# Kernel optimization log

Hardware: AMD Instinct MI355X
Metric: run time of the kernel (lower is better)

Reference implementation:

```python
import jax, jax.numpy as jnp
import numpy as np

D_MODEL = 1024
N_HEAD = 16
STRIDE = 16
HEAD_DIM = D_MODEL // N_HEAD
B, TQ, TK = 4, 2048, 8192
L = TK // STRIDE  # per-head key count (same for all heads since n_head <= stride and TK % stride == 0)


def setup_inputs() -> dict:
    key = jax.random.key(0)
    ks = jax.random.split(key, 12)
    w_scale = 0.02
    return {
        "q": jax.random.normal(ks[0], (B, TQ, D_MODEL), dtype=jnp.float32),
        "k": jax.random.normal(ks[1], (B, TK, D_MODEL), dtype=jnp.float32),
        "v": jax.random.normal(ks[2], (B, TK, D_MODEL), dtype=jnp.float32),
        "src_mask": jnp.ones((B, 1, 1, TK), dtype=jnp.int32),
        "w_q": jax.random.normal(ks[3], (D_MODEL, D_MODEL), dtype=jnp.float32) * w_scale,
        "b_q": jnp.zeros((D_MODEL,), dtype=jnp.float32),
        "w_k": jax.random.normal(ks[4], (D_MODEL, D_MODEL), dtype=jnp.float32) * w_scale,
        "b_k": jnp.zeros((D_MODEL,), dtype=jnp.float32),
        "w_v": jax.random.normal(ks[5], (D_MODEL, D_MODEL), dtype=jnp.float32) * w_scale,
        "b_v": jnp.zeros((D_MODEL,), dtype=jnp.float32),
        "w_o": jax.random.normal(ks[6], (D_MODEL, D_MODEL), dtype=jnp.float32) * w_scale,
        "b_o": jnp.zeros((D_MODEL,), dtype=jnp.float32),
    }


def reference(q, k, v, src_mask, w_q, b_q, w_k, b_k, w_v, b_v, w_o, b_o):
    # projections (torch Linear: x @ W.T + b)
    Q = (q @ w_q.T + b_q).reshape(B, TQ, N_HEAD, HEAD_DIM).transpose(0, 2, 1, 3)  # [B,H,Tq,D]
    K = (k @ w_k.T + b_k).reshape(B, TK, N_HEAD, HEAD_DIM).transpose(0, 2, 1, 3)  # [B,H,Tk,D]
    V = (v @ w_v.T + b_v).reshape(B, TK, N_HEAD, HEAD_DIM).transpose(0, 2, 1, 3)

    # HEPOS strided per-head key indices: head h attends to positions h, h+stride, ...
    idx = jnp.arange(N_HEAD)[:, None] + STRIDE * jnp.arange(L)[None, :]  # [H,L]
    gidx = idx[None, :, :, None]  # broadcastable over batch and head_dim
    Kh = jnp.take_along_axis(K, gidx, axis=2)  # [B,H,L,D]
    Vh = jnp.take_along_axis(V, gidx, axis=2)  # [B,H,L,D]

    scores = jnp.einsum("bhqd,bhld->bhql", Q, Kh) / jnp.sqrt(jnp.float32(HEAD_DIM))
    # gather per-head mask slice: src_mask [B,1,1,Tk] -> [B,H,1,L]
    mask_b = jnp.broadcast_to(src_mask, (B, N_HEAD, 1, TK))
    mask_h = jnp.take_along_axis(mask_b, idx[None, :, None, :], axis=3)  # [B,H,1,L]
    scores = jnp.where(mask_h == 0, jnp.float32(-1e9), scores)

    attn = jax.nn.softmax(scores, axis=-1)  # dropout is identity in eval mode
    out = jnp.einsum("bhql,bhld->bhqd", attn, Vh)  # [B,H,Tq,D]
    out = out.transpose(0, 2, 1, 3).reshape(B, TQ, D_MODEL)
    return out @ w_o.T + b_o
```

## Files before the change

kernel.cpp:

```cpp
#include <hip/hip_runtime.h>
#include <stdint.h>

#define NBATCH 4
#define TQ 2048
#define TKK 8192
#define DM 1024
#define HDIM 64
#define LLEN 512

typedef __bf16 bf16;
typedef __attribute__((ext_vector_type(4))) float f32x4;
typedef __attribute__((ext_vector_type(8))) __bf16 bf16x8;
typedef __attribute__((ext_vector_type(4))) __bf16 bf16x4;

typedef const __attribute__((address_space(1))) void* gas1_t;
typedef __attribute__((address_space(3))) void* las3_t;

__device__ __forceinline__ void gload_lds16(const void* g, void* l) {
  __builtin_amdgcn_global_load_lds((gas1_t)(uintptr_t)g, (las3_t)(uint32_t)(uintptr_t)l, 16, 0, 0);
}

__global__ void cast_f32_bf16(const float* __restrict__ src, bf16* __restrict__ dst, int n4) {
  int i = blockIdx.x * blockDim.x + threadIdx.x;
  int stride = gridDim.x * blockDim.x;
  for (; i < n4; i += stride) {
    float4 v = ((const float4*)src)[i];
    bf16x4 o;
    o[0] = (bf16)v.x; o[1] = (bf16)v.y; o[2] = (bf16)v.z; o[3] = (bf16)v.w;
    ((bf16x4*)dst)[i] = o;
  }
}

__global__ void build_maskf(const int* __restrict__ sm, float* __restrict__ mf) {
  int i = blockIdx.x * blockDim.x + threadIdx.x;
  int bh = i >> 9, l = i & 511;
  int b = bh >> 4, h = bh & 15;
  mf[i] = sm[b * TKK + h + 16 * l] ? 1.0f : 0.0f;
}

template<bool OUT_BF16>
__global__ __launch_bounds__(256) void gemm_bt_bias(
    const bf16* __restrict__ A, const bf16* __restrict__ Bm,
    const float* __restrict__ bias, void* __restrict__ Cout, float scale) {
  __shared__ bf16 As[128 * 64];
  __shared__ bf16 Bs[128 * 64];
  const int t = threadIdx.x;
  const int lane = t & 63, w = t >> 6;
  const int wm = w >> 1, wn = w & 1;
  const int m0 = blockIdx.y * 128, n0 = blockIdx.x * 128;
  const int c = lane & 15, g = lane >> 4;
  f32x4 acc[4][4] = {};
  for (int k0 = 0; k0 < DM; k0 += 64) {
    __syncthreads();
    #pragma unroll
    for (int i = 0; i < 4; ++i) {
      int chunk = i * 256 + t;
      int row = chunk >> 3, blk = chunk & 7;
      gload_lds16(A + (size_t)(m0 + row) * DM + k0 + blk * 8, As + chunk * 8);
      gload_lds16(Bm + (size_t)(n0 + row) * DM + k0 + blk * 8, Bs + chunk * 8);
    }
    __syncthreads();
    #pragma unroll
    for (int kk = 0; kk < 2; ++kk) {
      bf16x8 af[4], bfr[4];
      #pragma unroll
      for (int f = 0; f < 4; ++f)
        af[f] = *(const bf16x8*)(As + (wm * 64 + f * 16 + c) * 64 + kk * 32 + g * 8);
      #pragma unroll
      for (int f = 0; f < 4; ++f)
        bfr[f] = *(const bf16x8*)(Bs + (wn * 64 + f * 16 + c) * 64 + kk * 32 + g * 8);
      #pragma unroll
      for (int mi = 0; mi < 4; ++mi)
        #pragma unroll
        for (int ni = 0; ni < 4; ++ni)
          acc[mi][ni] = __builtin_amdgcn_mfma_f32_16x16x32_bf16(af[mi], bfr[ni], acc[mi][ni], 0, 0, 0);
    }
  }
  #pragma unroll
  for (int ni = 0; ni < 4; ++ni) {
    int n = n0 + wn * 64 + ni * 16 + c;
    float bv = bias[n];
    #pragma unroll
    for (int mi = 0; mi < 4; ++mi) {
      int m = m0 + wm * 64 + mi * 16 + g * 4;
      #pragma unroll
      for (int j = 0; j < 4; ++j) {
        float vv = (acc[mi][ni][j] + bv) * scale;
        if (OUT_BF16) ((bf16*)Cout)[(size_t)(m + j) * DM + n] = (bf16)vv;
        else          ((float*)Cout)[(size_t)(m + j) * DM + n] = vv;
      }
    }
  }
}

template<int TRANSPOSE>
__global__ __launch_bounds__(256) void kv_proj(
    const float* __restrict__ X, const bf16* __restrict__ W,
    const float* __restrict__ bias, bf16* __restrict__ Out) {
  __shared__ bf16 As[128 * 64];
  __shared__ bf16 Bs[64 * 64];
  const int t = threadIdx.x, lane = t & 63, w = t >> 6;
  const int wm = w >> 1, wn = w & 1;
  const int bh = blockIdx.y, b = bh >> 4, h = bh & 15;
  const int l0 = blockIdx.x * 128;
  const int c = lane & 15, g = lane >> 4;
  f32x4 acc[4][2] = {};
  for (int k0 = 0; k0 < DM; k0 += 64) {
    __syncthreads();
    #pragma unroll
    for (int i = 0; i < 8; ++i) {
      int chunk = i * 256 + t;
      int row = chunk >> 4, q4 = chunk & 15;
      float4 v = *(const float4*)(X + ((size_t)b * TKK + h + 16 * (l0 + row)) * DM + k0 + q4 * 4);
      bf16x4 o;
      o[0] = (bf16)v.x; o[1] = (bf16)v.y; o[2] = (bf16)v.z; o[3] = (bf16)v.w;
      uint32_t byte = (uint32_t)(row * 128 + q4 * 8) ^ (uint32_t)((row & 7) << 4);
      *(bf16x4*)((char*)As + byte) = o;
    }
    #pragma unroll
    for (int i = 0; i < 2; ++i) {
      int chunk = i * 256 + t;
      int row = chunk >> 3, blk = chunk & 7;
      uint4 v = *(const uint4*)(W + (size_t)(h * 64 + row) * DM + k0 + blk * 8);
      uint32_t byte = (uint32_t)(row * 128 + blk * 16) ^ (uint32_t)((row & 7) << 4);
      *(uint4*)((char*)Bs + byte) = v;
    }
    __syncthreads();
    #pragma unroll
    for (int kk = 0; kk < 2; ++kk) {
      bf16x8 af[4], bfr[2];
      #pragma unroll
      for (int f = 0; f < 4; ++f) {
        int row = wm * 64 + f * 16 + c;
        uint32_t byte = (uint32_t)(row * 128 + (kk * 32 + g * 8) * 2) ^ (uint32_t)((row & 7) << 4);
        af[f] = *(const bf16x8*)((char*)As + byte);
      }
      #pragma unroll
      for (int f = 0; f < 2; ++f) {
        int row = wn * 32 + f * 16 + c;
        uint32_t byte = (uint32_t)(row * 128 + (kk * 32 + g * 8) * 2) ^ (uint32_t)((row & 7) << 4);
        bfr[f] = *(const bf16x8*)((char*)Bs + byte);
      }
      #pragma unroll
      for (int mi = 0; mi < 4; ++mi)
        #pragma unroll
        for (int ni = 0; ni < 2; ++ni)
          acc[mi][ni] = __builtin_amdgcn_mfma_f32_16x16x32_bf16(af[mi], bfr[ni], acc[mi][ni], 0, 0, 0);
    }
  }
  #pragma unroll
  for (int ni = 0; ni < 2; ++ni) {
    int n = wn * 32 + ni * 16 + c;
    float bv = bias[h * 64 + n];
    #pragma unroll
    for (int mi = 0; mi < 4; ++mi) {
      int m = wm * 64 + mi * 16 + g * 4;
      if (TRANSPOSE == 0) {
        #pragma unroll
        for (int j = 0; j < 4; ++j)
          Out[((size_t)bh * LLEN + l0 + m + j) * 64 + n] = (bf16)(acc[mi][ni][j] + bv);
      } else {
        bf16x4 o;
        #pragma unroll
        for (int j = 0; j < 4; ++j) o[j] = (bf16)(acc[mi][ni][j] + bv);
        *(bf16x4*)(Out + ((size_t)bh * 64 + n) * LLEN + l0 + m) = o;
      }
    }
  }
}

__device__ __forceinline__ void stage_kv(const bf16* __restrict__ KH, const bf16* __restrict__ VT,
                                         bf16* Ks, bf16* Vs, int bh, int lt, int t) {
  #pragma unroll
  for (int i = 0; i < 4; ++i) {
    int chunk = i * 256 + t, row = chunk >> 3, blk = chunk & 7;
    uint4 v = *(const uint4*)(KH + ((size_t)bh * LLEN + lt * 128 + row) * 64 + blk * 8);
    uint32_t byte = (uint32_t)(row * 128 + blk * 16) ^ (uint32_t)((row & 7) << 4);
    *(uint4*)((char*)Ks + byte) = v;
  }
  #pragma unroll
  for (int i = 0; i < 4; ++i) {
    int chunk = i * 256 + t, row = chunk >> 4, blk = chunk & 15;
    uint4 v = *(const uint4*)(VT + ((size_t)bh * 64 + row) * LLEN + lt * 128 + blk * 8);
    uint32_t byte = (uint32_t)(row * 256 + blk * 16) ^ (uint32_t)((row & 7) << 4);
    *(uint4*)((char*)Vs + byte) = v;
  }
}

__global__ __launch_bounds__(256) void attn_kernel(
    const bf16* __restrict__ Qp, const bf16* __restrict__ KH, const bf16* __restrict__ VT,
    const float* __restrict__ maskf, bf16* __restrict__ AO) {
  __shared__ bf16 Qs[128 * 64];
  __shared__ bf16 Ks[128 * 64];
  __shared__ bf16 Vs[64 * 128];
  const int t = threadIdx.x, lane = t & 63, w = t >> 6;
  const int bh = blockIdx.y, b = bh >> 4, h = bh & 15;
  const int q0 = blockIdx.x * 128;
  const int c = lane & 15, g = lane >> 4;

  #pragma unroll
  for (int i = 0; i < 4; ++i) {
    int chunk = i * 256 + t, row = chunk >> 3, blk = chunk & 7;
    uint4 v = *(const uint4*)(Qp + ((size_t)(b * TQ + q0 + row)) * DM + h * 64 + blk * 8);
    uint32_t byte = (uint32_t)(row * 128 + blk * 16) ^ (uint32_t)((row & 7) << 4);
    *(uint4*)((char*)Qs + byte) = v;
  }
  stage_kv(KH, VT, Ks, Vs, bh, 0, t);
  __syncthreads();

  bf16x8 bq[2][2];
  #pragma unroll
  for (int nf = 0; nf < 2; ++nf)
    #pragma unroll
    for (int kk = 0; kk < 2; ++kk) {
      int row = w * 32 + nf * 16 + c;
      uint32_t byte = (uint32_t)(row * 128 + (kk * 32 + g * 8) * 2) ^ (uint32_t)((row & 7) << 4);
      bq[nf][kk] = *(const bf16x8*)((char*)Qs + byte);
    }

  float m_run[2] = {-1e30f, -1e30f};
  float l_run[2] = {0.0f, 0.0f};
  f32x4 acc_o[4][2] = {};

  #pragma unroll 1
  for (int lt = 0; lt < 4; ++lt) {
    f32x4 s[8][2] = {};
    #pragma unroll
    for (int kk = 0; kk < 2; ++kk) {
      bf16x8 ak[8];
      #pragma unroll
      for (int mf = 0; mf < 8; ++mf) {
        int row = mf * 16 + c;
        uint32_t byte = (uint32_t)(row * 128 + (kk * 32 + g * 8) * 2) ^ (uint32_t)((row & 7) << 4);
        ak[mf] = *(const bf16x8*)((char*)Ks + byte);
      }
      #pragma unroll
      for (int mf = 0; mf < 8; ++mf)
        #pragma unroll
        for (int nf = 0; nf < 2; ++nf)
          s[mf][nf] = __builtin_amdgcn_mfma_f32_16x16x32_bf16(ak[mf], bq[nf][kk], s[mf][nf], 0, 0, 0);
    }
    #pragma unroll
    for (int nf = 0; nf < 2; ++nf) {
      float mnew = m_run[nf];
      #pragma unroll
      for (int mf = 0; mf < 8; ++mf)
        #pragma unroll
        for (int j = 0; j < 4; ++j)
          mnew = fmaxf(mnew, s[mf][nf][j]);
      mnew = fmaxf(mnew, __shfl_xor(mnew, 16));
      mnew = fmaxf(mnew, __shfl_xor(mnew, 32));
      float fs = exp2f((m_run[nf] - mnew) * 1.44269504f);
      m_run[nf] = mnew;
      float rs = 0.0f;
      #pragma unroll
      for (int mf = 0; mf < 8; ++mf) {
        float4 mk = *(const float4*)(maskf + (size_t)bh * LLEN + lt * 128 + mf * 16 + 4 * g);
        #pragma unroll
        for (int j = 0; j < 4; ++j) {
          float p = exp2f((s[mf][nf][j] - mnew) * 1.44269504f) * ((const float*)&mk)[j];
          s[mf][nf][j] = p;
          rs += p;
        }
      }
      rs += __shfl_xor(rs, 16);
      rs += __shfl_xor(rs, 32);
      l_run[nf] = l_run[nf] * fs + rs;
      #pragma unroll
      for (int mf = 0; mf < 4; ++mf) acc_o[mf][nf] *= fs;
    }
    #pragma unroll
    for (int kk = 0; kk < 4; ++kk) {
      bf16x8 pb[2];
      #pragma unroll
      for (int nf = 0; nf < 2; ++nf)
        #pragma unroll
        for (int s8 = 0; s8 < 8; ++s8)
          pb[nf][s8] = (bf16)s[kk * 2 + (s8 >> 2)][nf][s8 & 3];
      #pragma unroll
      for (int mf = 0; mf < 4; ++mf) {
        int d = mf * 16 + c;
        uint32_t base = (uint32_t)(d * 256 + (kk * 32 + g * 4) * 2);
        uint32_t swz = (uint32_t)((d & 7) << 4);
        bf16x4 lo = *(const bf16x4*)((char*)Vs + (base ^ swz));
        bf16x4 hi = *(const bf16x4*)((char*)Vs + ((base + 32) ^ swz));
        bf16x8 av = __builtin_shufflevector(lo, hi, 0, 1, 2, 3, 4, 5, 6, 7);
        #pragma unroll
        for (int nf = 0; nf < 2; ++nf)
          acc_o[mf][nf] = __builtin_amdgcn_mfma_f32_16x16x32_bf16(av, pb[nf], acc_o[mf][nf], 0, 0, 0);
      }
    }
    if (lt < 3) {
      __syncthreads();
      stage_kv(KH, VT, Ks, Vs, bh, lt + 1, t);
      __syncthreads();
    }
  }
  #pragma unroll
  for (int nf = 0; nf < 2; ++nf) {
    float inv = 1.0f / l_run[nf];
    int qq = q0 + w * 32 + nf * 16 + c;
    #pragma unroll
    for (int mf = 0; mf < 4; ++mf) {
      bf16x4 o;
      #pragma unroll
      for (int j = 0; j < 4; ++j) o[j] = (bf16)(acc_o[mf][nf][j] * inv);
      *(bf16x4*)(AO + ((size_t)(b * TQ + qq)) * DM + h * 64 + mf * 16 + 4 * g) = o;
    }
  }
}

extern "C" void kernel_launch(void* const* d_in, const int* in_sizes, int n_in,
                              void* d_out, int out_size, void* d_ws, size_t ws_size,
                              hipStream_t stream) {
  const float* q   = (const float*)d_in[0];
  const float* k   = (const float*)d_in[1];
  const float* v   = (const float*)d_in[2];
  const int*  smk  = (const int*)d_in[3];
  const float* w_q = (const float*)d_in[4];
  const float* b_q = (const float*)d_in[5];
  const float* w_k = (const float*)d_in[6];
  const float* b_k = (const float*)d_in[7];
  const float* w_v = (const float*)d_in[8];
  const float* b_v = (const float*)d_in[9];
  const float* w_o = (const float*)d_in[10];
  const float* b_o = (const float*)d_in[11];
  float* out = (float*)d_out;

  bf16* WS  = (bf16*)d_ws;
  bf16* WQ  = WS;
  bf16* WK  = WQ + (1u << 20);
  bf16* WV  = WK + (1u << 20);
  bf16* WO  = WV + (1u << 20);
  bf16* QB  = WO + (1u << 20);
  bf16* QP  = QB + (8u << 20);
  bf16* KH  = QP + (8u << 20);
  bf16* VTT = KH + (2u << 20);
  bf16* AO  = VTT + (2u << 20);
  float* MF = (float*)(AO + (8u << 20));

  cast_f32_bf16<<<512, 256, 0, stream>>>(w_q, WQ, 262144);
  cast_f32_bf16<<<512, 256, 0, stream>>>(w_k, WK, 262144);
  cast_f32_bf16<<<512, 256, 0, stream>>>(w_v, WV, 262144);
  cast_f32_bf16<<<512, 256, 0, stream>>>(w_o, WO, 262144);
  cast_f32_bf16<<<2048, 256, 0, stream>>>(q, QB, 2097152);
  build_maskf<<<128, 256, 0, stream>>>(smk, MF);

  gemm_bt_bias<true><<<dim3(8, 64), 256, 0, stream>>>(QB, WQ, b_q, QP, 0.125f);
  kv_proj<0><<<dim3(4, 64), 256, 0, stream>>>(k, WK, b_k, KH);
  kv_proj<1><<<dim3(4, 64), 256, 0, stream>>>(v, WV, b_v, VTT);
  attn_kernel<<<dim3(16, 64), 256, 0, stream>>>(QP, KH, VTT, MF, AO);
  gemm_bt_bias<false><<<dim3(8, 64), 256, 0, stream>>>(AO, WO, b_o, out, 1.0f);
}
```

Baseline: 499.2 us.

## Fuse prep casts, merge K/V projections, swizzle block order, add MFMA priority

```diff
diff --git a/kernel.cpp b/kernel.cpp
--- a/kernel.cpp
+++ b/kernel.cpp
@@ -20,22 +20,31 @@
   __builtin_amdgcn_global_load_lds((gas1_t)(uintptr_t)g, (las3_t)(uint32_t)(uintptr_t)l, 16, 0, 0);
 }
 
-__global__ void cast_f32_bf16(const float* __restrict__ src, bf16* __restrict__ dst, int n4) {
-  int i = blockIdx.x * blockDim.x + threadIdx.x;
+__device__ __forceinline__ void cast4(const float* __restrict__ src, bf16* __restrict__ dst, int i) {
+  float4 v = ((const float4*)src)[i];
+  bf16x4 o;
+  o[0] = (bf16)v.x; o[1] = (bf16)v.y; o[2] = (bf16)v.z; o[3] = (bf16)v.w;
+  ((bf16x4*)dst)[i] = o;
+}
+
+__global__ void prep_kernel(const float* __restrict__ q,
+                            const float* __restrict__ wq, const float* __restrict__ wk,
+                            const float* __restrict__ wv, const float* __restrict__ wo,
+                            const int* __restrict__ sm,
+                            bf16* __restrict__ QB, bf16* __restrict__ WQ, bf16* __restrict__ WK,
+                            bf16* __restrict__ WV, bf16* __restrict__ WO, float* __restrict__ MF) {
+  int tid = blockIdx.x * blockDim.x + threadIdx.x;
   int stride = gridDim.x * blockDim.x;
-  for (; i < n4; i += stride) {
-    float4 v = ((const float4*)src)[i];
-    bf16x4 o;
-    o[0] = (bf16)v.x; o[1] = (bf16)v.y; o[2] = (bf16)v.z; o[3] = (bf16)v.w;
-    ((bf16x4*)dst)[i] = o;
-  }
-}
-
-__global__ void build_maskf(const int* __restrict__ sm, float* __restrict__ mf) {
-  int i = blockIdx.x * blockDim.x + threadIdx.x;
-  int bh = i >> 9, l = i & 511;
-  int b = bh >> 4, h = bh & 15;
-  mf[i] = sm[b * TKK + h + 16 * l] ? 1.0f : 0.0f;
+  for (int i = tid; i < 2097152; i += stride) cast4(q, QB, i);
+  for (int i = tid; i < 262144; i += stride) cast4(wq, WQ, i);
+  for (int i = tid; i < 262144; i += stride) cast4(wk, WK, i);
+  for (int i = tid; i < 262144; i += stride) cast4(wv, WV, i);
+  for (int i = tid; i < 262144; i += stride) cast4(wo, WO, i);
+  for (int i = tid; i < 32768; i += stride) {
+    int bh = i >> 9, l = i & 511;
+    int b = bh >> 4, h = bh & 15;
+    MF[i] = sm[b * TKK + h + 16 * l] ? 1.0f : 0.0f;
+  }
 }
 
 template<bool OUT_BF16>
@@ -47,7 +56,9 @@
   const int t = threadIdx.x;
   const int lane = t & 63, w = t >> 6;
   const int wm = w >> 1, wn = w & 1;
-  const int m0 = blockIdx.y * 128, n0 = blockIdx.x * 128;
+  const int bid = blockIdx.x;
+  const int swz = (bid & 7) * 64 + (bid >> 3);
+  const int m0 = (swz >> 3) * 128, n0 = (swz & 7) * 128;
   const int c = lane & 15, g = lane >> 4;
   f32x4 acc[4][4] = {};
   for (int k0 = 0; k0 < DM; k0 += 64) {
@@ -93,27 +104,36 @@
   }
 }
 
-template<int TRANSPOSE>
-__global__ __launch_bounds__(256) void kv_proj(
-    const float* __restrict__ X, const bf16* __restrict__ W,
-    const float* __restrict__ bias, bf16* __restrict__ Out) {
-  __shared__ bf16 As[128 * 64];
+__global__ __launch_bounds__(256) void kv_proj_fused(
+    const float* __restrict__ Xk, const float* __restrict__ Xv,
+    const bf16* __restrict__ WK, const bf16* __restrict__ WV,
+    const float* __restrict__ bk, const float* __restrict__ bv,
+    bf16* __restrict__ KH, bf16* __restrict__ VTT) {
+  __shared__ bf16 As[64 * 64];
   __shared__ bf16 Bs[64 * 64];
   const int t = threadIdx.x, lane = t & 63, w = t >> 6;
   const int wm = w >> 1, wn = w & 1;
-  const int bh = blockIdx.y, b = bh >> 4, h = bh & 15;
-  const int l0 = blockIdx.x * 128;
+  const int bid = blockIdx.x;
+  const int swz = (bid & 7) * 128 + (bid >> 3);
+  const int iz = swz >> 9;
+  const int bh = (swz >> 3) & 63;
+  const int ltile = swz & 7;
+  const int b = bh >> 4, h = bh & 15;
+  const int l0 = ltile * 64;
+  const float* __restrict__ X = iz ? Xv : Xk;
+  const bf16* __restrict__ W = iz ? WV : WK;
+  const float* __restrict__ bias = iz ? bv : bk;
   const int c = lane & 15, g = lane >> 4;
-  f32x4 acc[4][2] = {};
+  f32x4 acc[2][2] = {};
   for (int k0 = 0; k0 < DM; k0 += 64) {
     __syncthreads();
     #pragma unroll
-    for (int i = 0; i < 8; ++i) {
+    for (int i = 0; i < 4; ++i) {
       int chunk = i * 256 + t;
       int row = chunk >> 4, q4 = chunk & 15;
-      float4 v = *(const float4*)(X + ((size_t)b * TKK + h + 16 * (l0 + row)) * DM + k0 + q4 * 4);
+      float4 vv = *(const float4*)(X + ((size_t)b * TKK + h + 16 * (l0 + row)) * DM + k0 + q4 * 4);
       bf16x4 o;
-      o[0] = (bf16)v.x; o[1] = (bf16)v.y; o[2] = (bf16)v.z; o[3] = (bf16)v.w;
+      o[0] = (bf16)vv.x; o[1] = (bf16)vv.y; o[2] = (bf16)vv.z; o[3] = (bf16)vv.w;
       uint32_t byte = (uint32_t)(row * 128 + q4 * 8) ^ (uint32_t)((row & 7) << 4);
       *(bf16x4*)((char*)As + byte) = o;
     }
@@ -121,17 +141,17 @@
     for (int i = 0; i < 2; ++i) {
       int chunk = i * 256 + t;
       int row = chunk >> 3, blk = chunk & 7;
-      uint4 v = *(const uint4*)(W + (size_t)(h * 64 + row) * DM + k0 + blk * 8);
+      uint4 vv = *(const uint4*)(W + (size_t)(h * 64 + row) * DM + k0 + blk * 8);
       uint32_t byte = (uint32_t)(row * 128 + blk * 16) ^ (uint32_t)((row & 7) << 4);
-      *(uint4*)((char*)Bs + byte) = v;
+      *(uint4*)((char*)Bs + byte) = vv;
     }
     __syncthreads();
     #pragma unroll
     for (int kk = 0; kk < 2; ++kk) {
-      bf16x8 af[4], bfr[2];
-      #pragma unroll
-      for (int f = 0; f < 4; ++f) {
-        int row = wm * 64 + f * 16 + c;
+      bf16x8 af[2], bfr[2];
+      #pragma unroll
+      for (int f = 0; f < 2; ++f) {
+        int row = wm * 32 + f * 16 + c;
         uint32_t byte = (uint32_t)(row * 128 + (kk * 32 + g * 8) * 2) ^ (uint32_t)((row & 7) << 4);
         af[f] = *(const bf16x8*)((char*)As + byte);
       }
@@ -142,7 +162,7 @@
         bfr[f] = *(const bf16x8*)((char*)Bs + byte);
       }
       #pragma unroll
-      for (int mi = 0; mi < 4; ++mi)
+      for (int mi = 0; mi < 2; ++mi)
         #pragma unroll
         for (int ni = 0; ni < 2; ++ni)
           acc[mi][ni] = __builtin_amdgcn_mfma_f32_16x16x32_bf16(af[mi], bfr[ni], acc[mi][ni], 0, 0, 0);
@@ -151,19 +171,19 @@
   #pragma unroll
   for (int ni = 0; ni < 2; ++ni) {
     int n = wn * 32 + ni * 16 + c;
-    float bv = bias[h * 64 + n];
-    #pragma unroll
-    for (int mi = 0; mi < 4; ++mi) {
-      int m = wm * 64 + mi * 16 + g * 4;
-      if (TRANSPOSE == 0) {
+    float bvv = bias[h * 64 + n];
+    #pragma unroll
+    for (int mi = 0; mi < 2; ++mi) {
+      int m = wm * 32 + mi * 16 + g * 4;
+      if (iz == 0) {
         #pragma unroll
         for (int j = 0; j < 4; ++j)
-          Out[((size_t)bh * LLEN + l0 + m + j) * 64 + n] = (bf16)(acc[mi][ni][j] + bv);
+          KH[((size_t)bh * LLEN + l0 + m + j) * 64 + n] = (bf16)(acc[mi][ni][j] + bvv);
       } else {
         bf16x4 o;
         #pragma unroll
-        for (int j = 0; j < 4; ++j) o[j] = (bf16)(acc[mi][ni][j] + bv);
-        *(bf16x4*)(Out + ((size_t)bh * 64 + n) * LLEN + l0 + m) = o;
+        for (int j = 0; j < 4; ++j) o[j] = (bf16)(acc[mi][ni][j] + bvv);
+        *(bf16x4*)(VTT + ((size_t)bh * 64 + n) * LLEN + l0 + m) = o;
       }
     }
   }
@@ -194,8 +214,10 @@
   __shared__ bf16 Ks[128 * 64];
   __shared__ bf16 Vs[64 * 128];
   const int t = threadIdx.x, lane = t & 63, w = t >> 6;
-  const int bh = blockIdx.y, b = bh >> 4, h = bh & 15;
-  const int q0 = blockIdx.x * 128;
+  const int bid = blockIdx.x;
+  const int swz = (bid & 7) * 128 + (bid >> 3);
+  const int bh = swz >> 4, b = bh >> 4, h = bh & 15;
+  const int q0 = (swz & 15) * 128;
   const int c = lane & 15, g = lane >> 4;
 
   #pragma unroll
@@ -234,11 +256,13 @@
         uint32_t byte = (uint32_t)(row * 128 + (kk * 32 + g * 8) * 2) ^ (uint32_t)((row & 7) << 4);
         ak[mf] = *(const bf16x8*)((char*)Ks + byte);
       }
+      __builtin_amdgcn_s_setprio(1);
       #pragma unroll
       for (int mf = 0; mf < 8; ++mf)
         #pragma unroll
         for (int nf = 0; nf < 2; ++nf)
           s[mf][nf] = __builtin_amdgcn_mfma_f32_16x16x32_bf16(ak[mf], bq[nf][kk], s[mf][nf], 0, 0, 0);
+      __builtin_amdgcn_s_setprio(0);
     }
     #pragma unroll
     for (int nf = 0; nf < 2; ++nf) {
@@ -281,13 +305,15 @@
       for (int mf = 0; mf < 4; ++mf) {
         int d = mf * 16 + c;
         uint32_t base = (uint32_t)(d * 256 + (kk * 32 + g * 4) * 2);
-        uint32_t swz = (uint32_t)((d & 7) << 4);
-        bf16x4 lo = *(const bf16x4*)((char*)Vs + (base ^ swz));
-        bf16x4 hi = *(const bf16x4*)((char*)Vs + ((base + 32) ^ swz));
+        uint32_t swzb = (uint32_t)((d & 7) << 4);
+        bf16x4 lo = *(const bf16x4*)((char*)Vs + (base ^ swzb));
+        bf16x4 hi = *(const bf16x4*)((char*)Vs + ((base + 32) ^ swzb));
         bf16x8 av = __builtin_shufflevector(lo, hi, 0, 1, 2, 3, 4, 5, 6, 7);
+        __builtin_amdgcn_s_setprio(1);
         #pragma unroll
         for (int nf = 0; nf < 2; ++nf)
           acc_o[mf][nf] = __builtin_amdgcn_mfma_f32_16x16x32_bf16(av, pb[nf], acc_o[mf][nf], 0, 0, 0);
+        __builtin_amdgcn_s_setprio(0);
       }
     }
     if (lt < 3) {
@@ -339,16 +365,9 @@
   bf16* AO  = VTT + (2u << 20);
   float* MF = (float*)(AO + (8u << 20));
 
-  cast_f32_bf16<<<512, 256, 0, stream>>>(w_q, WQ, 262144);
-  cast_f32_bf16<<<512, 256, 0, stream>>>(w_k, WK, 262144);
-  cast_f32_bf16<<<512, 256, 0, stream>>>(w_v, WV, 262144);
-  cast_f32_bf16<<<512, 256, 0, stream>>>(w_o, WO, 262144);
-  cast_f32_bf16<<<2048, 256, 0, stream>>>(q, QB, 2097152);
-  build_maskf<<<128, 256, 0, stream>>>(smk, MF);
-
-  gemm_bt_bias<true><<<dim3(8, 64), 256, 0, stream>>>(QB, WQ, b_q, QP, 0.125f);
-  kv_proj<0><<<dim3(4, 64), 256, 0, stream>>>(k, WK, b_k, KH);
-  kv_proj<1><<<dim3(4, 64), 256, 0, stream>>>(v, WV, b_v, VTT);
-  attn_kernel<<<dim3(16, 64), 256, 0, stream>>>(QP, KH, VTT, MF, AO);
-  gemm_bt_bias<false><<<dim3(8, 64), 256, 0, stream>>>(AO, WO, b_o, out, 1.0f);
-}
+  prep_kernel<<<2048, 256, 0, stream>>>(q, w_q, w_k, w_v, w_o, smk, QB, WQ, WK, WV, WO, MF);
+  gemm_bt_bias<true><<<512, 256, 0, stream>>>(QB, WQ, b_q, QP, 0.125f);
+  kv_proj_fused<<<1024, 256, 0, stream>>>(k, v, WK, WV, b_k, b_v, KH, VTT);
+  attn_kernel<<<1024, 256, 0, stream>>>(QP, KH, VTT, MF, AO);
+  gemm_bt_bias<false><<<512, 256, 0, stream>>>(AO, WO, b_o, out, 1.0f);
+}
```

Result: no change. 504.9 us (+1.1%).
